# Performance work log

Measured on AMD Instinct MI355X. Metric: run time of the kernel, lower is better.

The kernel has to match this reference:

```python
import jax, jax.numpy as jnp
import numpy as np

NUM_HEADS = 32
NUM_KV_HEADS = 8
HEAD_DIM = 128
SEQ = 2048
MASK_BLOCK = 128  # diffusion-LM denoising block size


def setup_inputs() -> dict:
    key = jax.random.key(0)
    kq, kk, kv = jax.random.split(key, 3)
    q = jax.random.normal(kq, (SEQ, NUM_HEADS * HEAD_DIM), dtype=jnp.float32)
    k = jax.random.normal(kk, (SEQ, NUM_KV_HEADS * HEAD_DIM), dtype=jnp.float32)
    v = jax.random.normal(kv, (SEQ, NUM_KV_HEADS * HEAD_DIM), dtype=jnp.float32)
    # block-causal mask at MASK_BLOCK granularity: token_q attends to token_kv
    # iff block(token_kv) <= block(token_q). Every row has >=1 True entry.
    blk = jnp.arange(SEQ) // MASK_BLOCK
    block_mask = blk[None, :] <= blk[:, None]  # [S, S] bool
    return {"q": q, "k": k, "v": v, "block_mask": block_mask}


def reference(q, k, v, block_mask):
    S = q.shape[0]
    scale = 1.0 / np.sqrt(HEAD_DIM).astype(np.float32)  # flex_attention default scale
    qh = q.reshape(S, NUM_HEADS, HEAD_DIM)       # [S, Hq, D]
    kh = k.reshape(S, NUM_KV_HEADS, HEAD_DIM)    # [S, Hkv, D]
    vh = v.reshape(S, NUM_KV_HEADS, HEAD_DIM)
    # GQA: repeat each kv head over its query-head group
    group = NUM_HEADS // NUM_KV_HEADS
    kh = jnp.repeat(kh, group, axis=1)           # [S, Hq, D]
    vh = jnp.repeat(vh, group, axis=1)
    scores = jnp.einsum('qhd,khd->hqk', qh, kh) * scale  # [Hq, S, S]
    neg_inf = jnp.finfo(scores.dtype).min
    scores = jnp.where(block_mask[None, :, :], scores, neg_inf)
    probs = jax.nn.softmax(scores, axis=-1)
    o = jnp.einsum('hqk,khd->qhd', probs, vh)    # [S, Hq, D]
    return o.reshape(S, NUM_HEADS * HEAD_DIM)
```

## Files before the change

### kernel.cpp

```cpp
#include <hip/hip_runtime.h>
#include <hip/hip_bf16.h>

#define SEQL  2048
#define NHQ   32
#define NHKV  8
#define HD    128

typedef __attribute__((ext_vector_type(4))) float          f32x4;
typedef __attribute__((ext_vector_type(8))) short          bf16x8;
typedef __attribute__((ext_vector_type(4))) unsigned short u16x4;
typedef __attribute__((ext_vector_type(8))) unsigned short u16x8;
typedef __attribute__((ext_vector_type(2))) unsigned int   u32x2;

__device__ __forceinline__ unsigned short f2bf(float f) {
  union { float f; unsigned u; } v; v.f = f;
  unsigned u = v.u;
  return (unsigned short)((u + 0x7fffu + ((u >> 16) & 1u)) >> 16);
}

__device__ __forceinline__ unsigned cvtpk_bf16(float lo, float hi) {
  unsigned r;
  asm("v_cvt_pk_bf16_f32 %0, %1, %2" : "=v"(r) : "v"(lo), "v"(hi));
  return r;
}

__device__ __forceinline__ void gload16(const void* g, void* l) {
  __builtin_amdgcn_global_load_lds(
      (const __attribute__((address_space(1))) unsigned int*)g,
      (__attribute__((address_space(3))) unsigned int*)l, 16, 0, 0);
}

__global__ __launch_bounds__(256) void prep_k(const float* __restrict__ k,
                                              unsigned short* __restrict__ kws) {
  int t = blockIdx.x * 256 + threadIdx.x;
  int s   = t >> 7;
  int col = (t & 127) << 3;
  int hkv = col >> 7;
  int d0  = col & 127;
  const float* src = k + (size_t)s * (NHKV * HD) + col;
  f32x4 a = *(const f32x4*)src;
  f32x4 b = *(const f32x4*)(src + 4);
  u16x8 r;
  r[0] = f2bf(a[0]); r[1] = f2bf(a[1]); r[2] = f2bf(a[2]); r[3] = f2bf(a[3]);
  r[4] = f2bf(b[0]); r[5] = f2bf(b[1]); r[6] = f2bf(b[2]); r[7] = f2bf(b[3]);
  int tile = s >> 6, rr = s & 63;
  int idx = (rr * 128 + d0) ^ ((rr & 7) << 3);
  *(u16x8*)(kws + (((size_t)(hkv * 32 + tile)) << 13) + idx) = r;
}

__global__ __launch_bounds__(256) void prep_v(const float* __restrict__ v,
                                              unsigned short* __restrict__ vws) {
  int t = blockIdx.x * 256 + threadIdx.x;
  int d   = t & 127;
  int hkv = (t >> 7) & 7;
  int rg  = t >> 10;
  int s0  = rg << 3;
  const float* src = v + (size_t)s0 * (NHKV * HD) + hkv * HD + d;
  u16x8 r;
  #pragma unroll
  for (int j = 0; j < 8; ++j) r[j] = f2bf(src[(size_t)j * (NHKV * HD)]);
  int tile = rg >> 3;
  int rloc = (rg & 7) << 3;
  int idx = (d * 64 + rloc) ^ ((d & 7) << 3);
  *(u16x8*)(vws + (((size_t)(hkv * 32 + tile)) << 13) + idx) = r;
}

__global__ __launch_bounds__(256, 2) void attn_fwd4(
    const float* __restrict__ q,
    const unsigned short* __restrict__ kws,
    const unsigned short* __restrict__ vws,
    float* __restrict__ out)
{
  __shared__ unsigned short Kb[2][8192];
  __shared__ unsigned short Vb[2][8192];
  __shared__ unsigned int   Pst[4][512];

  const int tid  = threadIdx.x;
  const int lane = tid & 63;
  const int wv   = tid >> 6;
  const int l15  = lane & 15;
  const int lhi  = lane >> 4;
  const int swzP = (l15 & 7) << 2;
  const int swzK = (l15 & 7) << 3;

  const int bx   = blockIdx.x;
  const int hkv  = bx & 7;
  const int h    = hkv * 4 + ((bx >> 3) & 3);
  const int pr   = bx >> 5;
  const int qtA  = pr, qtB = 31 - pr;
  const int nA   = ((qtA >> 1) + 1) * 2;
  const int T    = 34;

  const float qscale = 0.08838834764831845f * 1.4426950408889634f;
  const float THR = 11.5f;

  const unsigned short* ktiles = kws + (((size_t)hkv * 32) << 13);
  const unsigned short* vtiles = vws + (((size_t)hkv * 32) << 13);

  bf16x8 qf[4];
  f32x4 oacc[8];
  float mrun, lrun;

  auto loadQ = [&](int qt) {
    const float* qbase = q + (size_t)(qt * 64 + wv * 16 + l15) * (NHQ * HD) + h * HD + lhi * 8;
    #pragma unroll
    for (int c = 0; c < 4; ++c) {
      f32x4 a = *(const f32x4*)(qbase + c * 32);
      f32x4 b = *(const f32x4*)(qbase + c * 32 + 4);
      bf16x8 r;
      r[0] = (short)f2bf(a[0] * qscale);
      r[1] = (short)f2bf(a[1] * qscale);
      r[2] = (short)f2bf(a[2] * qscale);
      r[3] = (short)f2bf(a[3] * qscale);
      r[4] = (short)f2bf(b[0] * qscale);
      r[5] = (short)f2bf(b[1] * qscale);
      r[6] = (short)f2bf(b[2] * qscale);
      r[7] = (short)f2bf(b[3] * qscale);
      qf[c] = r;
    }
  };

  auto resetAcc = [&]() {
    #pragma unroll
    for (int i = 0; i < 8; ++i) oacc[i] = (f32x4){0.f, 0.f, 0.f, 0.f};
    mrun = -1e30f; lrun = 0.f;
  };

  auto epilogue = [&](int qt) {
    float invl = 1.0f / lrun;
    float* ob = out + (size_t)(qt * 64 + wv * 16 + l15) * (NHQ * HD) + h * HD + lhi * 4;
    #pragma unroll
    for (int dsub = 0; dsub < 8; ++dsub)
      *(f32x4*)(ob + dsub * 16) = oacc[dsub] * invl;
  };

  auto STAGE = [&](int b, int kvt) {
    const char* gk = (const char*)(ktiles + ((size_t)kvt << 13));
    const char* gv = (const char*)(vtiles + ((size_t)kvt << 13));
    char* lk = (char*)&Kb[b][0];
    char* lv = (char*)&Vb[b][0];
    #pragma unroll
    for (int i = 0; i < 4; ++i) {
      const int off = wv * 4096 + i * 1024;
      gload16(gk + off + lane * 16, lk + off);
      gload16(gv + off + lane * 16, lv + off);
    }
  };

  auto compute = [&](int b) {
    f32x4 sa[4];
    __builtin_amdgcn_s_setprio(1);
    #pragma unroll
    for (int sub = 0; sub < 4; ++sub) {
      f32x4 acc = (f32x4){0.f, 0.f, 0.f, 0.f};
      const int row = sub * 16 + l15;
      #pragma unroll
      for (int c = 0; c < 4; ++c) {
        bf16x8 kf = *(const bf16x8*)(&Kb[b][(row * 128 + c * 32 + lhi * 8) ^ swzK]);
        acc = __builtin_amdgcn_mfma_f32_16x16x32_bf16(kf, qf[c], acc, 0, 0, 0);
      }
      sa[sub] = acc;
    }
    __builtin_amdgcn_s_setprio(0);
    float mt = -1e30f;
    #pragma unroll
    for (int sub = 0; sub < 4; ++sub)
      #pragma unroll
      for (int r = 0; r < 4; ++r) mt = fmaxf(mt, sa[sub][r]);
    mt = fmaxf(mt, __shfl_xor(mt, 16));
    mt = fmaxf(mt, __shfl_xor(mt, 32));
    if (__any(mt > mrun + THR)) {
      float mn = fmaxf(mrun, mt);
      float c0 = exp2f(mrun - mn);
      mrun = mn; lrun *= c0;
      #pragma unroll
      for (int d = 0; d < 8; ++d) oacc[d] *= c0;
    }
    {
      float ts = 0.f;
      #pragma unroll
      for (int sub = 0; sub < 4; ++sub) {
        float p0 = exp2f(sa[sub][0] - mrun);
        float p1 = exp2f(sa[sub][1] - mrun);
        float p2 = exp2f(sa[sub][2] - mrun);
        float p3 = exp2f(sa[sub][3] - mrun);
        ts += (p0 + p1) + (p2 + p3);
        u32x2 w;
        w[0] = cvtpk_bf16(p0, p1);
        w[1] = cvtpk_bf16(p2, p3);
        *(u32x2*)(&Pst[wv][(l15 * 32 + sub * 8 + lhi * 2) ^ swzP]) = w;
      }
      ts += __shfl_xor(ts, 16);
      ts += __shfl_xor(ts, 32);
      lrun += ts;
    }
    __builtin_amdgcn_s_setprio(1);
    #pragma unroll
    for (int kc = 0; kc < 2; ++kc) {
      bf16x8 pf = *(const bf16x8*)(&Pst[wv][(l15 * 32 + kc * 16 + lhi * 4) ^ swzP]);
      #pragma unroll
      for (int dsub = 0; dsub < 8; ++dsub) {
        const int d = dsub * 16 + l15;
        bf16x8 vf = *(const bf16x8*)(&Vb[b][(d * 64 + kc * 32 + lhi * 8) ^ swzK]);
        oacc[dsub] = __builtin_amdgcn_mfma_f32_16x16x32_bf16(vf, pf, oacc[dsub], 0, 0, 0);
      }
    }
    __builtin_amdgcn_s_setprio(0);
  };

  loadQ(qtA);
  resetAcc();
  STAGE(0, 0);
  int buf = 0;
  for (int t = 0; t < T; ++t) {
    if (t == nA) { epilogue(qtA); loadQ(qtB); resetAcc(); }
    if (t + 1 < T) {
      const int p = t + 1;
      STAGE(buf ^ 1, (p < nA) ? p : p - nA);
      asm volatile("s_waitcnt vmcnt(8)" ::: "memory");
    } else {
      asm volatile("s_waitcnt vmcnt(0)" ::: "memory");
    }
    __builtin_amdgcn_s_barrier();
    asm volatile("" ::: "memory");
    compute(buf);
    asm volatile("" ::: "memory");
    __builtin_amdgcn_s_barrier();
    buf ^= 1;
  }
  epilogue(qtB);
}

__global__ __launch_bounds__(256) void attn_v1(
    const float* __restrict__ q,
    const float* __restrict__ k,
    const float* __restrict__ v,
    float* __restrict__ out)
{
  __shared__ unsigned short Ks[64 * 128];
  __shared__ unsigned short Vt[128 * 64];
  __shared__ unsigned short Psl[4][16 * 64];

  const int tid  = threadIdx.x;
  const int lane = tid & 63;
  const int wv   = tid >> 6;
  const int bx   = blockIdx.x;
  const int h    = bx & 31;
  const int qt   = (SEQL / 64 - 1) - (bx >> 5);
  const int q0   = qt * 64;
  const int hkv  = h >> 2;
  const int l15 = lane & 15;
  const int lhi = lane >> 4;
  const float qscale = 0.08838834764831845f * 1.4426950408889634f;

  bf16x8 qf[4];
  {
    const float* qbase = q + (size_t)(q0 + wv * 16 + l15) * (NHQ * HD) + h * HD + lhi * 8;
    #pragma unroll
    for (int c = 0; c < 4; ++c) {
      const float* p8 = qbase + c * 32;
      f32x4 a = *(const f32x4*)p8;
      f32x4 b = *(const f32x4*)(p8 + 4);
      bf16x8 r;
      r[0] = (short)f2bf(a[0] * qscale); r[1] = (short)f2bf(a[1] * qscale);
      r[2] = (short)f2bf(a[2] * qscale); r[3] = (short)f2bf(a[3] * qscale);
      r[4] = (short)f2bf(b[0] * qscale); r[5] = (short)f2bf(b[1] * qscale);
      r[6] = (short)f2bf(b[2] * qscale); r[7] = (short)f2bf(b[3] * qscale);
      qf[c] = r;
    }
  }
  f32x4 oacc[8];
  #pragma unroll
  for (int i = 0; i < 8; ++i) oacc[i] = (f32x4){0.f, 0.f, 0.f, 0.f};
  float mrun[4], lrun[4];
  #pragma unroll
  for (int r = 0; r < 4; ++r) { mrun[r] = -1e30f; lrun[r] = 0.f; }
  const int ntiles = ((q0 >> 7) + 1) * 2;
  for (int t = 0; t < ntiles; ++t) {
    const int kv0 = t * 64;
    __syncthreads();
    #pragma unroll
    for (int it = 0; it < 8; ++it) {
      int c = it * 256 + tid;
      int row = c >> 5;
      int dc = (c & 31) << 2;
      f32x4 x = *(const f32x4*)(k + (size_t)(kv0 + row) * (NHKV * HD) + hkv * HD + dc);
      u16x4 y;
      y[0] = f2bf(x[0]); y[1] = f2bf(x[1]); y[2] = f2bf(x[2]); y[3] = f2bf(x[3]);
      int idx = (row * HD + dc) ^ ((row & 7) << 3);
      *(u16x4*)(&Ks[idx]) = y;
    }
    {
      int row = tid >> 2;
      int db = (tid & 3) << 5;
      const float* vbase = v + (size_t)(kv0 + row) * (NHKV * HD) + hkv * HD + db;
      #pragma unroll
      for (int it = 0; it < 8; ++it) {
        f32x4 x = *(const f32x4*)(vbase + it * 4);
        int d0 = db + it * 4;
        #pragma unroll
        for (int j = 0; j < 4; ++j) {
          int d = d0 + j;
          int idx = (d * 64 + row) ^ ((d & 7) << 3);
          Vt[idx] = f2bf(x[j]);
        }
      }
    }
    __syncthreads();
    f32x4 sacc[4];
    #pragma unroll
    for (int sub = 0; sub < 4; ++sub) {
      f32x4 acc = (f32x4){0.f, 0.f, 0.f, 0.f};
      #pragma unroll
      for (int c = 0; c < 4; ++c) {
        int row = sub * 16 + l15;
        int idx = (row * HD + c * 32 + lhi * 8) ^ ((row & 7) << 3);
        bf16x8 kf = *(const bf16x8*)(&Ks[idx]);
        acc = __builtin_amdgcn_mfma_f32_16x16x32_bf16(qf[c], kf, acc, 0, 0, 0);
      }
      sacc[sub] = acc;
    }
    float corr[4];
    #pragma unroll
    for (int r = 0; r < 4; ++r) {
      float mt = fmaxf(fmaxf(sacc[0][r], sacc[1][r]), fmaxf(sacc[2][r], sacc[3][r]));
      #pragma unroll
      for (int off = 1; off < 16; off <<= 1) mt = fmaxf(mt, __shfl_xor(mt, off));
      float mnew = fmaxf(mrun[r], mt);
      corr[r] = exp2f(mrun[r] - mnew);
      mrun[r] = mnew;
      float p0 = exp2f(sacc[0][r] - mnew);
      float p1 = exp2f(sacc[1][r] - mnew);
      float p2 = exp2f(sacc[2][r] - mnew);
      float p3 = exp2f(sacc[3][r] - mnew);
      int qr = (lhi << 2) + r;
      int swz = (qr & 7) << 3;
      int bq = qr * 64;
      Psl[wv][(bq + 0  + l15) ^ swz] = f2bf(p0);
      Psl[wv][(bq + 16 + l15) ^ swz] = f2bf(p1);
      Psl[wv][(bq + 32 + l15) ^ swz] = f2bf(p2);
      Psl[wv][(bq + 48 + l15) ^ swz] = f2bf(p3);
      float ts = p0 + p1 + p2 + p3;
      #pragma unroll
      for (int off = 1; off < 16; off <<= 1) ts += __shfl_xor(ts, off);
      lrun[r] = lrun[r] * corr[r] + ts;
    }
    #pragma unroll
    for (int dsub = 0; dsub < 8; ++dsub) {
      f32x4 o = oacc[dsub];
      o[0] *= corr[0]; o[1] *= corr[1]; o[2] *= corr[2]; o[3] *= corr[3];
      oacc[dsub] = o;
    }
    #pragma unroll
    for (int kc = 0; kc < 2; ++kc) {
      int pidx = (l15 * 64 + kc * 32 + lhi * 8) ^ ((l15 & 7) << 3);
      bf16x8 pf = *(const bf16x8*)(&Psl[wv][pidx]);
      #pragma unroll
      for (int dsub = 0; dsub < 8; ++dsub) {
        int d = dsub * 16 + l15;
        int vidx = (d * 64 + kc * 32 + lhi * 8) ^ ((d & 7) << 3);
        bf16x8 vf = *(const bf16x8*)(&Vt[vidx]);
        oacc[dsub] = __builtin_amdgcn_mfma_f32_16x16x32_bf16(pf, vf, oacc[dsub], 0, 0, 0);
      }
    }
  }
  float inv[4];
  #pragma unroll
  for (int r = 0; r < 4; ++r) inv[r] = 1.0f / lrun[r];
  float* obase = out + (size_t)(q0 + wv * 16 + (lhi << 2)) * (NHQ * HD) + h * HD + l15;
  #pragma unroll
  for (int dsub = 0; dsub < 8; ++dsub) {
    #pragma unroll
    for (int r = 0; r < 4; ++r) {
      obase[(size_t)r * (NHQ * HD) + dsub * 16] = oacc[dsub][r] * inv[r];
    }
  }
}

extern "C" void kernel_launch(void* const* d_in, const int* in_sizes, int n_in,
                              void* d_out, int out_size, void* d_ws, size_t ws_size,
                              hipStream_t stream) {
  const float* q = (const float*)d_in[0];
  const float* k = (const float*)d_in[1];
  const float* v = (const float*)d_in[2];
  float* out = (float*)d_out;
  const size_t need = (size_t)8 * 1024 * 1024 + 512;
  if (ws_size >= need) {
    unsigned short* kws = (unsigned short*)d_ws;
    unsigned short* vws = kws + (size_t)4 * 1024 * 1024 / 2;
    prep_k<<<1024, 256, 0, stream>>>(k, kws);
    prep_v<<<1024, 256, 0, stream>>>(v, vws);
    attn_fwd4<<<512, 256, 0, stream>>>(q, kws, vws, out);
  } else {
    attn_v1<<<1024, 256, 0, stream>>>(q, k, v, out);
  }
}
```

Measured before the change: 87.19 us.

## Drop LDS double buffering in favor of higher occupancy per CU

Replaces the double-buffered K/V shared-memory staging with a single buffer: each iteration loads the current tile, waits for all loads and barriers before computing. LDS per block roughly halves and launch bounds go from 2 to 4 blocks per CU, relying on inter-block overlap instead of intra-block prefetch. This risks exposing global load latency within each block and may pressure registers under the tighter launch bound. The grid has only 512 blocks, so higher occupancy may leave CUs underfilled.

```diff
diff --git a/kernel.cpp b/kernel.cpp
--- a/kernel.cpp
+++ b/kernel.cpp
@@ -65,14 +65,14 @@
   *(u16x8*)(vws + (((size_t)(hkv * 32 + tile)) << 13) + idx) = r;
 }
 
-__global__ __launch_bounds__(256, 2) void attn_fwd4(
+__global__ __launch_bounds__(256, 4) void attn_fwd5(
     const float* __restrict__ q,
     const unsigned short* __restrict__ kws,
     const unsigned short* __restrict__ vws,
     float* __restrict__ out)
 {
-  __shared__ unsigned short Kb[2][8192];
-  __shared__ unsigned short Vb[2][8192];
+  __shared__ unsigned short Kb[8192];
+  __shared__ unsigned short Vb[8192];
   __shared__ unsigned int   Pst[4][512];
 
   const int tid  = threadIdx.x;
@@ -134,11 +134,11 @@
       *(f32x4*)(ob + dsub * 16) = oacc[dsub] * invl;
   };
 
-  auto STAGE = [&](int b, int kvt) {
+  auto STAGE = [&](int kvt) {
     const char* gk = (const char*)(ktiles + ((size_t)kvt << 13));
     const char* gv = (const char*)(vtiles + ((size_t)kvt << 13));
-    char* lk = (char*)&Kb[b][0];
-    char* lv = (char*)&Vb[b][0];
+    char* lk = (char*)&Kb[0];
+    char* lv = (char*)&Vb[0];
     #pragma unroll
     for (int i = 0; i < 4; ++i) {
       const int off = wv * 4096 + i * 1024;
@@ -147,7 +147,7 @@
     }
   };
 
-  auto compute = [&](int b) {
+  auto compute = [&]() {
     f32x4 sa[4];
     __builtin_amdgcn_s_setprio(1);
     #pragma unroll
@@ -156,7 +156,7 @@
       const int row = sub * 16 + l15;
       #pragma unroll
       for (int c = 0; c < 4; ++c) {
-        bf16x8 kf = *(const bf16x8*)(&Kb[b][(row * 128 + c * 32 + lhi * 8) ^ swzK]);
+        bf16x8 kf = *(const bf16x8*)(&Kb[(row * 128 + c * 32 + lhi * 8) ^ swzK]);
         acc = __builtin_amdgcn_mfma_f32_16x16x32_bf16(kf, qf[c], acc, 0, 0, 0);
       }
       sa[sub] = acc;
@@ -201,7 +201,7 @@
       #pragma unroll
       for (int dsub = 0; dsub < 8; ++dsub) {
         const int d = dsub * 16 + l15;
-        bf16x8 vf = *(const bf16x8*)(&Vb[b][(d * 64 + kc * 32 + lhi * 8) ^ swzK]);
+        bf16x8 vf = *(const bf16x8*)(&Vb[(d * 64 + kc * 32 + lhi * 8) ^ swzK]);
         oacc[dsub] = __builtin_amdgcn_mfma_f32_16x16x32_bf16(vf, pf, oacc[dsub], 0, 0, 0);
       }
     }
@@ -210,23 +210,15 @@
 
   loadQ(qtA);
   resetAcc();
-  STAGE(0, 0);
-  int buf = 0;
   for (int t = 0; t < T; ++t) {
     if (t == nA) { epilogue(qtA); loadQ(qtB); resetAcc(); }
-    if (t + 1 < T) {
-      const int p = t + 1;
-      STAGE(buf ^ 1, (p < nA) ? p : p - nA);
-      asm volatile("s_waitcnt vmcnt(8)" ::: "memory");
-    } else {
-      asm volatile("s_waitcnt vmcnt(0)" ::: "memory");
-    }
+    STAGE((t < nA) ? t : t - nA);
+    asm volatile("s_waitcnt vmcnt(0)" ::: "memory");
     __builtin_amdgcn_s_barrier();
     asm volatile("" ::: "memory");
-    compute(buf);
+    compute();
     asm volatile("" ::: "memory");
     __builtin_amdgcn_s_barrier();
-    buf ^= 1;
   }
   epilogue(qtB);
 }
@@ -390,7 +382,7 @@
     unsigned short* vws = kws + (size_t)4 * 1024 * 1024 / 2;
     prep_k<<<1024, 256, 0, stream>>>(k, kws);
     prep_v<<<1024, 256, 0, stream>>>(v, vws);
-    attn_fwd4<<<512, 256, 0, stream>>>(q, kws, vws, out);
+    attn_fwd5<<<512, 256, 0, stream>>>(q, kws, vws, out);
   } else {
     attn_v1<<<1024, 256, 0, stream>>>(q, k, v, out);
   }
```

Result: no change. 88.08 us (+1.0%).

## Load V fragments directly from global into registers instead of LDS staging

Applied to the files above, without the earlier changes.

Drops the shared-memory double buffer for V tiles. Each wave now reads its V MFMA fragments straight from the pre-swizzled global workspace into registers at the start of compute, so these loads can overlap the QK^T MFMAs and softmax. LDS use and the async copy count per stage fall, and the waitcnt threshold is adjusted to match. The cost is that every wave re-reads the same V tile from global/L2 with no cross-wave sharing, a load latency that is exposed inside compute, and higher register pressure (16 bf16x8 values) under the 2-blocks-per-CU launch bound. It also reorders the row-max reduction into a tree.

```diff
diff --git a/kernel.cpp b/kernel.cpp
--- a/kernel.cpp
+++ b/kernel.cpp
@@ -65,14 +65,13 @@
   *(u16x8*)(vws + (((size_t)(hkv * 32 + tile)) << 13) + idx) = r;
 }
 
-__global__ __launch_bounds__(256, 2) void attn_fwd4(
+__global__ __launch_bounds__(256, 2) void attn_fwd7(
     const float* __restrict__ q,
     const unsigned short* __restrict__ kws,
     const unsigned short* __restrict__ vws,
     float* __restrict__ out)
 {
   __shared__ unsigned short Kb[2][8192];
-  __shared__ unsigned short Vb[2][8192];
   __shared__ unsigned int   Pst[4][512];
 
   const int tid  = threadIdx.x;
@@ -136,18 +135,26 @@
 
   auto STAGE = [&](int b, int kvt) {
     const char* gk = (const char*)(ktiles + ((size_t)kvt << 13));
-    const char* gv = (const char*)(vtiles + ((size_t)kvt << 13));
     char* lk = (char*)&Kb[b][0];
-    char* lv = (char*)&Vb[b][0];
     #pragma unroll
     for (int i = 0; i < 4; ++i) {
       const int off = wv * 4096 + i * 1024;
       gload16(gk + off + lane * 16, lk + off);
-      gload16(gv + off + lane * 16, lv + off);
     }
   };
 
-  auto compute = [&](int b) {
+  auto compute = [&](int b, int kvt) {
+    bf16x8 vr[2][8];
+    {
+      const unsigned short* vt = vtiles + ((size_t)kvt << 13);
+      #pragma unroll
+      for (int kc = 0; kc < 2; ++kc)
+        #pragma unroll
+        for (int dsub = 0; dsub < 8; ++dsub) {
+          const int d = dsub * 16 + l15;
+          vr[kc][dsub] = *(const bf16x8*)(&vt[(d * 64 + kc * 32 + lhi * 8) ^ swzK]);
+        }
+    }
     f32x4 sa[4];
     __builtin_amdgcn_s_setprio(1);
     #pragma unroll
@@ -162,11 +169,11 @@
       sa[sub] = acc;
     }
     __builtin_amdgcn_s_setprio(0);
-    float mt = -1e30f;
-    #pragma unroll
-    for (int sub = 0; sub < 4; ++sub)
-      #pragma unroll
-      for (int r = 0; r < 4; ++r) mt = fmaxf(mt, sa[sub][r]);
+    float m0 = fmaxf(fmaxf(sa[0][0], sa[0][1]), fmaxf(sa[0][2], sa[0][3]));
+    float m1 = fmaxf(fmaxf(sa[1][0], sa[1][1]), fmaxf(sa[1][2], sa[1][3]));
+    float m2 = fmaxf(fmaxf(sa[2][0], sa[2][1]), fmaxf(sa[2][2], sa[2][3]));
+    float m3 = fmaxf(fmaxf(sa[3][0], sa[3][1]), fmaxf(sa[3][2], sa[3][3]));
+    float mt = fmaxf(fmaxf(m0, m1), fmaxf(m2, m3));
     mt = fmaxf(mt, __shfl_xor(mt, 16));
     mt = fmaxf(mt, __shfl_xor(mt, 32));
     if (__any(mt > mrun + THR)) {
@@ -200,9 +207,7 @@
       bf16x8 pf = *(const bf16x8*)(&Pst[wv][(l15 * 32 + kc * 16 + lhi * 4) ^ swzP]);
       #pragma unroll
       for (int dsub = 0; dsub < 8; ++dsub) {
-        const int d = dsub * 16 + l15;
-        bf16x8 vf = *(const bf16x8*)(&Vb[b][(d * 64 + kc * 32 + lhi * 8) ^ swzK]);
-        oacc[dsub] = __builtin_amdgcn_mfma_f32_16x16x32_bf16(vf, pf, oacc[dsub], 0, 0, 0);
+        oacc[dsub] = __builtin_amdgcn_mfma_f32_16x16x32_bf16(vr[kc][dsub], pf, oacc[dsub], 0, 0, 0);
       }
     }
     __builtin_amdgcn_s_setprio(0);
@@ -213,17 +218,18 @@
   STAGE(0, 0);
   int buf = 0;
   for (int t = 0; t < T; ++t) {
+    const int kvt = (t < nA) ? t : t - nA;
     if (t == nA) { epilogue(qtA); loadQ(qtB); resetAcc(); }
     if (t + 1 < T) {
       const int p = t + 1;
       STAGE(buf ^ 1, (p < nA) ? p : p - nA);
-      asm volatile("s_waitcnt vmcnt(8)" ::: "memory");
+      asm volatile("s_waitcnt vmcnt(4)" ::: "memory");
     } else {
       asm volatile("s_waitcnt vmcnt(0)" ::: "memory");
     }
     __builtin_amdgcn_s_barrier();
     asm volatile("" ::: "memory");
-    compute(buf);
+    compute(buf, kvt);
     asm volatile("" ::: "memory");
     __builtin_amdgcn_s_barrier();
     buf ^= 1;
@@ -390,7 +396,7 @@
     unsigned short* vws = kws + (size_t)4 * 1024 * 1024 / 2;
     prep_k<<<1024, 256, 0, stream>>>(k, kws);
     prep_v<<<1024, 256, 0, stream>>>(v, vws);
-    attn_fwd4<<<512, 256, 0, stream>>>(q, kws, vws, out);
+    attn_fwd7<<<512, 256, 0, stream>>>(q, kws, vws, out);
   } else {
     attn_v1<<<1024, 256, 0, stream>>>(q, k, v, out);
   }
```

Result: slower. 109.1 us (+25.1%).

## Keep softmax probabilities in registers by permuting V tile layout to match MFMA

Applied to the files above, without the earlier changes.

The P matrix is no longer round-tripped through per-wave shared memory. The V workspace is reordered in prep_v so that the key ordering matches the register layout of the QK^T accumulator, which lets packed bf16 probabilities feed the PV MFMA directly as operands. This removes LDS stores and loads plus their latency from the inner loop, and frees the Pst shared buffer. The max reduction is also rebalanced into a tree. Correctness now depends on the permuted key ordering being the same in the V layout and the P fragment.

```diff
diff --git a/kernel.cpp b/kernel.cpp
--- a/kernel.cpp
+++ b/kernel.cpp
@@ -10,7 +10,6 @@
 typedef __attribute__((ext_vector_type(8))) short          bf16x8;
 typedef __attribute__((ext_vector_type(4))) unsigned short u16x4;
 typedef __attribute__((ext_vector_type(8))) unsigned short u16x8;
-typedef __attribute__((ext_vector_type(2))) unsigned int   u32x2;
 
 __device__ __forceinline__ unsigned short f2bf(float f) {
   union { float f; unsigned u; } v; v.f = f;
@@ -51,21 +50,25 @@
 __global__ __launch_bounds__(256) void prep_v(const float* __restrict__ v,
                                               unsigned short* __restrict__ vws) {
   int t = blockIdx.x * 256 + threadIdx.x;
-  int d   = t & 127;
-  int hkv = (t >> 7) & 7;
-  int rg  = t >> 10;
-  int s0  = rg << 3;
+  int d    = t & 127;
+  int hkv  = (t >> 7) & 7;
+  int rest = t >> 10;
+  int tile = rest >> 3;
+  int g    = (rest >> 2) & 1;
+  int lhi  = rest & 3;
+  int s0   = tile * 64 + g * 32 + lhi * 4;
   const float* src = v + (size_t)s0 * (NHKV * HD) + hkv * HD + d;
   u16x8 r;
   #pragma unroll
-  for (int j = 0; j < 8; ++j) r[j] = f2bf(src[(size_t)j * (NHKV * HD)]);
-  int tile = rg >> 3;
-  int rloc = (rg & 7) << 3;
-  int idx = (d * 64 + rloc) ^ ((d & 7) << 3);
+  for (int j = 0; j < 8; ++j) {
+    int soff = ((j >> 2) << 4) + (j & 3);
+    r[j] = f2bf(src[(size_t)soff * (NHKV * HD)]);
+  }
+  int idx = (d * 64 + g * 32 + lhi * 8) ^ ((d & 7) << 3);
   *(u16x8*)(vws + (((size_t)(hkv * 32 + tile)) << 13) + idx) = r;
 }
 
-__global__ __launch_bounds__(256, 2) void attn_fwd4(
+__global__ __launch_bounds__(256, 2) void attn_fwd8(
     const float* __restrict__ q,
     const unsigned short* __restrict__ kws,
     const unsigned short* __restrict__ vws,
@@ -73,14 +76,12 @@
 {
   __shared__ unsigned short Kb[2][8192];
   __shared__ unsigned short Vb[2][8192];
-  __shared__ unsigned int   Pst[4][512];
 
   const int tid  = threadIdx.x;
   const int lane = tid & 63;
   const int wv   = tid >> 6;
   const int l15  = lane & 15;
   const int lhi  = lane >> 4;
-  const int swzP = (l15 & 7) << 2;
   const int swzK = (l15 & 7) << 3;
 
   const int bx   = blockIdx.x;
@@ -162,11 +163,11 @@
       sa[sub] = acc;
     }
     __builtin_amdgcn_s_setprio(0);
-    float mt = -1e30f;
-    #pragma unroll
-    for (int sub = 0; sub < 4; ++sub)
-      #pragma unroll
-      for (int r = 0; r < 4; ++r) mt = fmaxf(mt, sa[sub][r]);
+    float m0 = fmaxf(fmaxf(sa[0][0], sa[0][1]), fmaxf(sa[0][2], sa[0][3]));
+    float m1 = fmaxf(fmaxf(sa[1][0], sa[1][1]), fmaxf(sa[1][2], sa[1][3]));
+    float m2 = fmaxf(fmaxf(sa[2][0], sa[2][1]), fmaxf(sa[2][2], sa[2][3]));
+    float m3 = fmaxf(fmaxf(sa[3][0], sa[3][1]), fmaxf(sa[3][2], sa[3][3]));
+    float mt = fmaxf(fmaxf(m0, m1), fmaxf(m2, m3));
     mt = fmaxf(mt, __shfl_xor(mt, 16));
     mt = fmaxf(mt, __shfl_xor(mt, 32));
     if (__any(mt > mrun + THR)) {
@@ -176,6 +177,7 @@
       #pragma unroll
       for (int d = 0; d < 8; ++d) oacc[d] *= c0;
     }
+    unsigned pw[8];
     {
       float ts = 0.f;
       #pragma unroll
@@ -185,10 +187,8 @@
         float p2 = exp2f(sa[sub][2] - mrun);
         float p3 = exp2f(sa[sub][3] - mrun);
         ts += (p0 + p1) + (p2 + p3);
-        u32x2 w;
-        w[0] = cvtpk_bf16(p0, p1);
-        w[1] = cvtpk_bf16(p2, p3);
-        *(u32x2*)(&Pst[wv][(l15 * 32 + sub * 8 + lhi * 2) ^ swzP]) = w;
+        pw[2 * sub]     = cvtpk_bf16(p0, p1);
+        pw[2 * sub + 1] = cvtpk_bf16(p2, p3);
       }
       ts += __shfl_xor(ts, 16);
       ts += __shfl_xor(ts, 32);
@@ -197,7 +197,12 @@
     __builtin_amdgcn_s_setprio(1);
     #pragma unroll
     for (int kc = 0; kc < 2; ++kc) {
-      bf16x8 pf = *(const bf16x8*)(&Pst[wv][(l15 * 32 + kc * 16 + lhi * 4) ^ swzP]);
+      union { unsigned u[4]; bf16x8 v8; } pk;
+      pk.u[0] = pw[4 * kc + 0];
+      pk.u[1] = pw[4 * kc + 1];
+      pk.u[2] = pw[4 * kc + 2];
+      pk.u[3] = pw[4 * kc + 3];
+      bf16x8 pf = pk.v8;
       #pragma unroll
       for (int dsub = 0; dsub < 8; ++dsub) {
         const int d = dsub * 16 + l15;
@@ -390,7 +395,7 @@
     unsigned short* vws = kws + (size_t)4 * 1024 * 1024 / 2;
     prep_k<<<1024, 256, 0, stream>>>(k, kws);
     prep_v<<<1024, 256, 0, stream>>>(v, vws);
-    attn_fwd4<<<512, 256, 0, stream>>>(q, kws, vws, out);
+    attn_fwd8<<<512, 256, 0, stream>>>(q, kws, vws, out);
   } else {
     attn_v1<<<1024, 256, 0, stream>>>(q, k, v, out);
   }
```

Result: no change. 88.65 us (+1.7%).
